# Kernel optimization log

Measured on AMD Instinct MI355X. Metric: run time of the kernel, lower is better.

Reference implementation:

```python
import jax, jax.numpy as jnp
import numpy as np

STRIDE = 1
PADDING = 1
GROUPS = 1


def setup_inputs() -> dict:
    key = jax.random.key(0)
    kx, kw, kb = jax.random.split(key, 3)
    x_int = jax.random.randint(kx, (16, 256, 56, 56), 0, 127, dtype=jnp.int32)
    weight_int = jax.random.randint(kw, (256, 256, 3, 3), 0, 127, dtype=jnp.int32)
    bias_int = jax.random.randint(kb, (256,), 0, 127, dtype=jnp.int32)
    return {"x_int": x_int, "weight_int": weight_int, "bias_int": bias_int}


def reference(x_int, weight_int, bias_int):
    # Integer conv2d with int32 accumulation, exactly F.conv2d semantics.
    y = jax.lax.conv_general_dilated(
        x_int,
        weight_int,
        window_strides=(STRIDE, STRIDE),
        padding=((PADDING, PADDING), (PADDING, PADDING)),
        dimension_numbers=("NCHW", "OIHW", "NCHW"),
        feature_group_count=GROUPS,
    )
    # bias broadcast over [B, Cout, H, W]
    return y + bias_int[None, :, None, None]
```

## Files before the change

kernel.cpp:

```cpp
#include <hip/hip_runtime.h>


typedef int v4i  __attribute__((ext_vector_type(4)));
typedef int v16i __attribute__((ext_vector_type(16)));

#define X8_ROWSTRIDE 1856
#define X8_IMGSTRIDE 107648
#define X8_BYTES     13778944
#define W8_CHUNK     18432

typedef const __attribute__((address_space(1))) unsigned char* gptr_t;
typedef __attribute__((address_space(3))) unsigned char* lptr_t;

__device__ __forceinline__ int pack4(const int* p, int stride) {
  return (p[0] & 255) | ((p[stride] & 255) << 8) |
         ((p[2 * stride] & 255) << 16) | ((p[3 * stride] & 255) << 24);
}

__global__ __launch_bounds__(256)
void pack_all(const int* __restrict__ x, const int* __restrict__ wgt,
              unsigned char* __restrict__ ws8) {
  const int g = blockIdx.x * 256 + threadIdx.x;
  if (g < 861184) {
    const int p = g & 1;
    int t = g >> 1;
    const int slot = t % 58; t /= 58;
    const int row  = t % 58;
    const int cb   = t / 58;
    v4i v = (v4i){0, 0, 0, 0};
    if (row >= 1 && row <= 56 && slot >= 1 && slot <= 56) {
      const int chunk = cb >> 4, b = cb & 15;
      const int srcg = (p + slot) & 1;
      const int ci0 = chunk * 32 + srcg * 16;
      const int* src = x + (b * 256 + ci0) * 3136 + (row - 1) * 56 + (slot - 1);
      v = (v4i){pack4(src, 3136), pack4(src + 4 * 3136, 3136),
                pack4(src + 8 * 3136, 3136), pack4(src + 12 * 3136, 3136)};
    }
    *(v4i*)(ws8 + (cb * 58 + row) * X8_ROWSTRIDE + slot * 32 + p * 16) = v;
  } else {
    const int gw = g - 861184;
    const int p = gw & 1;
    int t = gw >> 1;
    const int tap = t % 9;  t /= 9;
    const int co = t & 63;
    const int tcc = t >> 6;
    const int chunk = tcc & 7, cotile = tcc >> 3;
    const int srcg = (p + co) & 1;
    const int ci0 = chunk * 32 + srcg * 16;
    const int* src = wgt + ((cotile * 64 + co) * 256 + ci0) * 9 + tap;
    v4i v = (v4i){pack4(src, 9), pack4(src + 36, 9),
                  pack4(src + 72, 9), pack4(src + 108, 9)};
    *(v4i*)(ws8 + X8_BYTES + (t * 9 + tap) * 32 + p * 16) = v;
  }
}

__global__ __launch_bounds__(128, 2)
void conv_main(const unsigned char* __restrict__ ws8, const int* __restrict__ bias,
               int* __restrict__ out) {
  __shared__ __align__(16) unsigned char lds[18432 + 12288];
  __shared__ int bls[64];
  unsigned char* wls = lds;
  unsigned char* xs  = lds + 18432;

  const int tid = threadIdx.x, lane = tid & 63, wv = tid >> 6;
  const int n = lane & 31, gq = lane >> 5;
  const int tc = blockIdx.x;
  const int h0 = blockIdx.y * 4;
  const int b  = blockIdx.z;

  if (tid < 64) bls[tid] = bias[tc * 64 + tid];

  const int abase = n * 288 + (((gq + n) & 1) << 4);
  int boff[3][4];
  #pragma unroll
  for (int kw = 0; kw < 3; ++kw)
    #pragma unroll
    for (int bt = 0; bt < 4; ++bt) {
      int slot = bt * 16 + (n & 15) + kw;
      if (slot > 57) slot = 57;
      boff[kw][bt] = slot * 32 + (((gq + slot) & 1) << 4);
    }
  const int rbase = (2 * wv + (n >> 4)) * X8_ROWSTRIDE;

  v16i acc[2][4];
  #pragma unroll
  for (int i = 0; i < 2; ++i)
    #pragma unroll
    for (int j = 0; j < 4; ++j)
      acc[i][j] = (v16i){0,0,0,0,0,0,0,0,0,0,0,0,0,0,0,0};

  const unsigned char* wg = ws8 + X8_BYTES + tc * (8 * W8_CHUNK);
  const unsigned char* xg = ws8 + b * X8_IMGSTRIDE + h0 * X8_ROWSTRIDE;

  for (int c = 0; c < 8; ++c) {
    __syncthreads();
    const gptr_t wsrc = (gptr_t)(wg + c * W8_CHUNK);
    #pragma unroll
    for (int i = 0; i < 9; ++i)
      __builtin_amdgcn_global_load_lds(wsrc + i * 2048 + tid * 16,
                                       (lptr_t)(wls + i * 2048 + tid * 16), 16, 0, 0);
    const gptr_t xsrc = (gptr_t)(xg + c * (16 * X8_IMGSTRIDE));
    #pragma unroll
    for (int i = 0; i < 6; ++i)
      __builtin_amdgcn_global_load_lds(xsrc + i * 2048 + tid * 16,
                                       (lptr_t)(xs + i * 2048 + tid * 16), 16, 0, 0);
    __syncthreads();
    #pragma unroll
    for (int kh = 0; kh < 3; ++kh) {
      const unsigned char* xr = xs + rbase + kh * X8_ROWSTRIDE;
      #pragma unroll
      for (int kw = 0; kw < 3; ++kw) {
        const int tap = kh * 3 + kw;
        const v4i a0 = *(const v4i*)(wls + abase + tap * 32);
        const v4i a1 = *(const v4i*)(wls + 9216 + abase + tap * 32);
        #pragma unroll
        for (int bt = 0; bt < 4; ++bt) {
          const v4i bb = *(const v4i*)(xr + boff[kw][bt]);
          acc[0][bt] = __builtin_amdgcn_mfma_i32_32x32x32_i8(a0, bb, acc[0][bt], 0, 0, 0);
          acc[1][bt] = __builtin_amdgcn_mfma_i32_32x32x32_i8(a1, bb, acc[1][bt], 0, 0, 0);
        }
      }
    }
  }

  const int h = h0 + 2 * wv + (n >> 4);
  const int wbase = lane & 15;
  #pragma unroll
  for (int ct = 0; ct < 2; ++ct) {
    #pragma unroll
    for (int r = 0; r < 16; ++r) {
      const int co64 = ct * 32 + (r & 3) + 8 * (r >> 2) + 4 * gq;
      const int bv = bls[co64];
      int* orow = out + ((b * 256 + tc * 64 + co64) * 56 + h) * 56;
      #pragma unroll
      for (int bt = 0; bt < 4; ++bt) {
        const int w0 = bt * 16 + wbase;
        if (w0 < 56) orow[w0] = acc[ct][bt][r] + bv;
      }
    }
  }
}

extern "C" void kernel_launch(void* const* d_in, const int* in_sizes, int n_in,
                              void* d_out, int out_size, void* d_ws, size_t ws_size,
                              hipStream_t stream) {
  const int* x    = (const int*)d_in[0];
  const int* w    = (const int*)d_in[1];
  const int* bias = (const int*)d_in[2];
  unsigned char* ws8 = (unsigned char*)d_ws;
  hipLaunchKernelGGL(pack_all, dim3(3508), dim3(256), 0, stream, x, w, ws8);
  hipLaunchKernelGGL(conv_main, dim3(4, 14, 16), dim3(128), 0, stream,
                     ws8, bias, (int*)d_out);
}
```

Before: 135.9 us.

## Double-buffer LDS staging and enlarge conv blocks to 14 output rows

Each conv block now runs 512 threads, with 7 compute waves covering 14 output rows instead of 4, so every weight chunk loaded into LDS is reused across more rows. LDS holds two weight and input buffers, so chunk c+1 is loaded asynchronously while chunk c is computed, needing only one barrier per chunk. The grid shrinks to 256 blocks, about one per CU. The LDS footprint roughly triples and one wave only helps with loading, which may limit occupancy and leave load balance across CUs fragile.

```diff
diff --git a/kernel.cpp b/kernel.cpp
--- a/kernel.cpp
+++ b/kernel.cpp
@@ -8,6 +8,8 @@
 #define X8_IMGSTRIDE 107648
 #define X8_BYTES     13778944
 #define W8_CHUNK     18432
+#define XS_OFF       36864
+#define XS_BUF       30720
 
 typedef const __attribute__((address_space(1))) unsigned char* gptr_t;
 typedef __attribute__((address_space(3))) unsigned char* lptr_t;
@@ -54,19 +56,41 @@
   }
 }
 
-__global__ __launch_bounds__(128, 2)
+__device__ __forceinline__ void stage_chunk(const unsigned char* wg,
+                                            const unsigned char* xg,
+                                            unsigned char* ldsb, int c, int tid) {
+  const unsigned char* wsrc = wg + c * W8_CHUNK;
+  unsigned char* wdst = ldsb + (c & 1) * W8_CHUNK;
+  __builtin_amdgcn_global_load_lds((gptr_t)(wsrc + tid * 16),
+                                   (lptr_t)(wdst + tid * 16), 16, 0, 0);
+  __builtin_amdgcn_global_load_lds((gptr_t)(wsrc + 8192 + tid * 16),
+                                   (lptr_t)(wdst + 8192 + tid * 16), 16, 0, 0);
+  if (tid < 128)
+    __builtin_amdgcn_global_load_lds((gptr_t)(wsrc + 16384 + tid * 16),
+                                     (lptr_t)(wdst + 16384 + tid * 16), 16, 0, 0);
+  const unsigned char* xsrc = xg + c * (16 * X8_IMGSTRIDE);
+  unsigned char* xdst = ldsb + XS_OFF + (c & 1) * XS_BUF;
+  #pragma unroll
+  for (int i = 0; i < 3; ++i)
+    __builtin_amdgcn_global_load_lds((gptr_t)(xsrc + i * 8192 + tid * 16),
+                                     (lptr_t)(xdst + i * 8192 + tid * 16), 16, 0, 0);
+  if (tid < 384)
+    __builtin_amdgcn_global_load_lds((gptr_t)(xsrc + 24576 + tid * 16),
+                                     (lptr_t)(xdst + 24576 + tid * 16), 16, 0, 0);
+}
+
+__global__ __launch_bounds__(512, 2)
 void conv_main(const unsigned char* __restrict__ ws8, const int* __restrict__ bias,
                int* __restrict__ out) {
-  __shared__ __align__(16) unsigned char lds[18432 + 12288];
+  __shared__ __align__(16) unsigned char lds[2 * W8_CHUNK + 2 * XS_BUF];
   __shared__ int bls[64];
-  unsigned char* wls = lds;
-  unsigned char* xs  = lds + 18432;
 
   const int tid = threadIdx.x, lane = tid & 63, wv = tid >> 6;
   const int n = lane & 31, gq = lane >> 5;
-  const int tc = blockIdx.x;
-  const int h0 = blockIdx.y * 4;
-  const int b  = blockIdx.z;
+  const int tc = blockIdx.y;
+  const int hb = blockIdx.x;
+  const int hg = hb >> 4, b = hb & 15;
+  const int h0 = hg * 14;
 
   if (tid < 64) bls[tid] = bias[tc * 64 + tid];
 
@@ -92,37 +116,33 @@
   const unsigned char* wg = ws8 + X8_BYTES + tc * (8 * W8_CHUNK);
   const unsigned char* xg = ws8 + b * X8_IMGSTRIDE + h0 * X8_ROWSTRIDE;
 
+  stage_chunk(wg, xg, lds, 0, tid);
   for (int c = 0; c < 8; ++c) {
     __syncthreads();
-    const gptr_t wsrc = (gptr_t)(wg + c * W8_CHUNK);
-    #pragma unroll
-    for (int i = 0; i < 9; ++i)
-      __builtin_amdgcn_global_load_lds(wsrc + i * 2048 + tid * 16,
-                                       (lptr_t)(wls + i * 2048 + tid * 16), 16, 0, 0);
-    const gptr_t xsrc = (gptr_t)(xg + c * (16 * X8_IMGSTRIDE));
-    #pragma unroll
-    for (int i = 0; i < 6; ++i)
-      __builtin_amdgcn_global_load_lds(xsrc + i * 2048 + tid * 16,
-                                       (lptr_t)(xs + i * 2048 + tid * 16), 16, 0, 0);
-    __syncthreads();
-    #pragma unroll
-    for (int kh = 0; kh < 3; ++kh) {
-      const unsigned char* xr = xs + rbase + kh * X8_ROWSTRIDE;
+    if (c < 7) stage_chunk(wg, xg, lds, c + 1, tid);
+    if (wv < 7) {
+      const unsigned char* wls = lds + (c & 1) * W8_CHUNK;
+      const unsigned char* xs  = lds + XS_OFF + (c & 1) * XS_BUF;
       #pragma unroll
-      for (int kw = 0; kw < 3; ++kw) {
-        const int tap = kh * 3 + kw;
-        const v4i a0 = *(const v4i*)(wls + abase + tap * 32);
-        const v4i a1 = *(const v4i*)(wls + 9216 + abase + tap * 32);
+      for (int kh = 0; kh < 3; ++kh) {
+        const unsigned char* xr = xs + rbase + kh * X8_ROWSTRIDE;
         #pragma unroll
-        for (int bt = 0; bt < 4; ++bt) {
-          const v4i bb = *(const v4i*)(xr + boff[kw][bt]);
-          acc[0][bt] = __builtin_amdgcn_mfma_i32_32x32x32_i8(a0, bb, acc[0][bt], 0, 0, 0);
-          acc[1][bt] = __builtin_amdgcn_mfma_i32_32x32x32_i8(a1, bb, acc[1][bt], 0, 0, 0);
+        for (int kw = 0; kw < 3; ++kw) {
+          const int tap = kh * 3 + kw;
+          const v4i a0 = *(const v4i*)(wls + abase + tap * 32);
+          const v4i a1 = *(const v4i*)(wls + 9216 + abase + tap * 32);
+          #pragma unroll
+          for (int bt = 0; bt < 4; ++bt) {
+            const v4i bb = *(const v4i*)(xr + boff[kw][bt]);
+            acc[0][bt] = __builtin_amdgcn_mfma_i32_32x32x32_i8(a0, bb, acc[0][bt], 0, 0, 0);
+            acc[1][bt] = __builtin_amdgcn_mfma_i32_32x32x32_i8(a1, bb, acc[1][bt], 0, 0, 0);
+          }
         }
       }
     }
   }
 
+  if (wv >= 7) return;
   const int h = h0 + 2 * wv + (n >> 4);
   const int wbase = lane & 15;
   #pragma unroll
@@ -149,6 +169,6 @@
   const int* bias = (const int*)d_in[2];
   unsigned char* ws8 = (unsigned char*)d_ws;
   hipLaunchKernelGGL(pack_all, dim3(3508), dim3(256), 0, stream, x, w, ws8);
-  hipLaunchKernelGGL(conv_main, dim3(4, 14, 16), dim3(128), 0, stream,
+  hipLaunchKernelGGL(conv_main, dim3(64, 4, 1), dim3(512), 0, stream,
                      ws8, bias, (int*)d_out);
 }
```

Result: faster. 131.5 us (-3.3%).
